# Kernel optimization log

Measured on AMD Instinct MI355X. Metric: run time of the kernel, lower is better.

## Reference

```python
import jax, jax.numpy as jnp
import numpy as np

N = 100000   # num nodes
E = 640000   # num edges
IN, H, OUT = 6, 128, 1
BN_EPS = 1e-5


def setup_inputs() -> dict:
    key = jax.random.key(0)
    ks = jax.random.split(key, 12)
    x = jax.random.normal(ks[0], (N, IN), dtype=jnp.float32)
    edge_index = jax.random.randint(ks[1], (2, E), 0, N, dtype=jnp.int64)
    def lin(k, fin, fout):
        s = 1.0 / np.sqrt(fin)
        return jax.random.uniform(k, (fin, fout), jnp.float32, -s, s)
    return {
        "x": x,
        "edge_index": edge_index,
        "W1": lin(ks[2], IN, H),  "b1": jnp.zeros((H,), jnp.float32),
        "W2": lin(ks[3], H, H),   "b2": jnp.zeros((H,), jnp.float32),
        "W3": lin(ks[4], H, OUT), "b3": jnp.zeros((OUT,), jnp.float32),
        "g1": jnp.ones((H,), jnp.float32),  "be1": jnp.zeros((H,), jnp.float32),
        "g2": jnp.ones((H,), jnp.float32),  "be2": jnp.zeros((H,), jnp.float32),
    }


def _gcn_norm(edge_index):
    # add self-loops, then symmetric normalization D^-1/2 (A+I) D^-1/2
    loop = jnp.arange(N, dtype=edge_index.dtype)
    src = jnp.concatenate([edge_index[0], loop])
    dst = jnp.concatenate([edge_index[1], loop])
    deg = jax.ops.segment_sum(jnp.ones_like(dst, dtype=jnp.float32), dst, num_segments=N)
    dis = jnp.where(deg > 0, jax.lax.rsqrt(deg), 0.0)
    norm = dis[src] * dis[dst]  # (E+N,)
    return src, dst, norm


def _conv(h, W, b, src, dst, norm):
    m = h @ W                                   # (N, out) linear transform first
    msg = m[src] * norm[:, None]                # gather + edge scaling
    return jax.ops.segment_sum(msg, dst, num_segments=N) + b


def _bn(h, g, be):
    mu = h.mean(axis=0)
    var = h.var(axis=0)  # biased, as torch BN uses for normalization
    return g * (h - mu) * jax.lax.rsqrt(var + BN_EPS) + be


def reference(x, edge_index, W1, b1, W2, b2, W3, b3, g1, be1, g2, be2):
    src, dst, norm = _gcn_norm(edge_index)
    h = jax.nn.relu(_bn(_conv(x, W1, b1, src, dst, norm), g1, be1))
    h = jax.nn.relu(_bn(_conv(h, W2, b2, src, dst, norm), g2, be2))
    out = _conv(h, W3, b3, src, dst, norm)
    return jax.nn.sigmoid(out)  # (N, 1) risk scores
```

## Files before the change

### kernel.cpp

```cpp
#include <hip/hip_runtime.h>
#include <hip/hip_bf16.h>
#include <math.h>

#define HDIM 128
#define BN_EPS 1e-5f
#define CHUNK 512
#define TM 64
#define LDA 132

__device__ __forceinline__ int eget(const void* ei, long long pos, int is64) {
    return is64 ? (int)((const long long*)ei)[pos] : ((const int*)ei)[pos];
}
__device__ __forceinline__ unsigned short f2bf(float f) {
    unsigned int u = __float_as_uint(f);
    u += 0x7fffu + ((u >> 16) & 1u);
    return (unsigned short)(u >> 16);
}
__device__ __forceinline__ float bflo(unsigned int u) {
    return __uint_as_float(u << 16);
}
__device__ __forceinline__ float bfhi(unsigned int u) {
    return __uint_as_float(u & 0xffff0000u);
}

__global__ void k_detect(const int* ei32, int* flag) {
    if (threadIdx.x == 0) {
        int nz = 0;
        for (int k = 0; k < 64; ++k) nz += (ei32[2 * k + 1] != 0);
        *flag = (nz < 8) ? 1 : 0;
    }
}

__global__ void k_count(const void* ei, const int* flag, int* cnt, int E) {
    int e = blockIdx.x * blockDim.x + threadIdx.x;
    if (e < E) {
        int d = eget(ei, (long long)E + e, *flag);
        atomicAdd(&cnt[d], 1);
    }
}

__global__ void k_dis(const int* cnt, float* dis, int N) {
    int i = blockIdx.x * blockDim.x + threadIdx.x;
    if (i < N) dis[i] = rsqrtf((float)(cnt[i] + 1));
}

__global__ void k_scan1(const int* cnt, int* bsum, int N) {
    __shared__ int s[256];
    int t = threadIdx.x;
    int i = blockIdx.x * CHUNK + t;
    int v = 0;
    if (i < N) v += cnt[i];
    if (i + 256 < N && t + 256 < CHUNK) v += cnt[i + 256];
    s[t] = v; __syncthreads();
    for (int o = 128; o > 0; o >>= 1) {
        if (t < o) s[t] += s[t + o];
        __syncthreads();
    }
    if (t == 0) bsum[blockIdx.x] = s[0];
}

__global__ void k_scan2(int* bsum, int nb) {
    __shared__ int s[512];
    int t = threadIdx.x;
    int carry = 0;
    for (int base = 0; base < nb; base += 512) {
        int i = base + t;
        int v = (i < nb) ? bsum[i] : 0;
        s[t] = v; __syncthreads();
        for (int o = 1; o < 512; o <<= 1) {
            int add = (t >= o) ? s[t - o] : 0;
            __syncthreads();
            s[t] += add;
            __syncthreads();
        }
        if (i < nb) bsum[i] = carry + s[t] - v;
        carry += s[511];
        __syncthreads();
    }
}

__global__ void k_scan3(const int* cnt, const int* bsum, int* rowptr, int N) {
    __shared__ int s[CHUNK];
    int t = threadIdx.x;
    int i = blockIdx.x * CHUNK + t;
    int v = (i < N) ? cnt[i] : 0;
    s[t] = v; __syncthreads();
    for (int o = 1; o < CHUNK; o <<= 1) {
        int add = (t >= o) ? s[t - o] : 0;
        __syncthreads();
        s[t] += add;
        __syncthreads();
    }
    if (i < N) rowptr[i] = bsum[blockIdx.x] + s[t] - v;
    if (i == N - 1) rowptr[N] = bsum[blockIdx.x] + s[t];
}

__global__ void k_fillcsr(const void* ei, const int* flag, const float* dis,
                          const int* rowptr, int* fill, int* esrc, float* enorm, int E) {
    int e = blockIdx.x * blockDim.x + threadIdx.x;
    if (e < E) {
        int is64 = *flag;
        int s = eget(ei, e, is64);
        int d = eget(ei, (long long)E + e, is64);
        int pos = rowptr[d] + atomicAdd(&fill[d], 1);
        esrc[pos] = s;
        enorm[pos] = dis[s] * dis[d];
    }
}

__global__ void k_padx(const float* __restrict__ x, float* __restrict__ xp, int N) {
    int t = blockIdx.x * blockDim.x + threadIdx.x;
    if (t < N * 8) {
        int i = t >> 3, c = t & 7;
        xp[t] = (c < 6) ? x[i * 6 + c] : 0.f;
    }
}

__global__ void k_gath_x(const float* __restrict__ xp, const int* __restrict__ rowptr,
                         const int* __restrict__ esrc, const float* __restrict__ enorm,
                         const float* __restrict__ dis, float* __restrict__ aggx, int N) {
    int i = blockIdx.x * blockDim.x + threadIdx.x;
    if (i >= N) return;
    float d = dis[i], d2 = d * d;
    float4 A = *(const float4*)&xp[i * 8];
    float2 B = *(const float2*)&xp[i * 8 + 4];
    float a0 = A.x * d2, a1 = A.y * d2, a2 = A.z * d2;
    float a3 = A.w * d2, a4 = B.x * d2, a5 = B.y * d2;
    int p = rowptr[i], pe = rowptr[i + 1];
    for (; p + 2 <= pe; p += 2) {
        int s0 = esrc[p], s1 = esrc[p + 1];
        float n0 = enorm[p], n1 = enorm[p + 1];
        float4 A0 = *(const float4*)&xp[s0 * 8];
        float2 B0 = *(const float2*)&xp[s0 * 8 + 4];
        float4 A1 = *(const float4*)&xp[s1 * 8];
        float2 B1 = *(const float2*)&xp[s1 * 8 + 4];
        a0 += A0.x * n0 + A1.x * n1; a1 += A0.y * n0 + A1.y * n1;
        a2 += A0.z * n0 + A1.z * n1; a3 += A0.w * n0 + A1.w * n1;
        a4 += B0.x * n0 + B1.x * n1; a5 += B0.y * n0 + B1.y * n1;
    }
    if (p < pe) {
        int s0 = esrc[p]; float n0 = enorm[p];
        float4 A0 = *(const float4*)&xp[s0 * 8];
        float2 B0 = *(const float2*)&xp[s0 * 8 + 4];
        a0 += A0.x * n0; a1 += A0.y * n0; a2 += A0.z * n0;
        a3 += A0.w * n0; a4 += B0.x * n0; a5 += B0.y * n0;
    }
    aggx[i * 6 + 0] = a0; aggx[i * 6 + 1] = a1; aggx[i * 6 + 2] = a2;
    aggx[i * 6 + 3] = a3; aggx[i * 6 + 4] = a4; aggx[i * 6 + 5] = a5;
}

__global__ void k_gemm6(const float* __restrict__ aggx, const float* __restrict__ W1,
                        const float* __restrict__ b1, unsigned short* __restrict__ out,
                        float* __restrict__ S, int N) {
    __shared__ float w[6 * HDIM];
    __shared__ float bb[HDIM];
    __shared__ float sh1[256], sh2[256];
    for (int t = threadIdx.x; t < 6 * HDIM; t += blockDim.x) w[t] = W1[t];
    if (threadIdx.x < HDIM) bb[threadIdx.x] = b1[threadIdx.x];
    __syncthreads();
    int j = threadIdx.x & (HDIM - 1);
    int sub = threadIdx.x >> 7;
    float s1 = 0.f, s2 = 0.f;
    for (long long i = blockIdx.x * 2 + sub; i < N; i += (long long)gridDim.x * 2) {
        const float* r = &aggx[i * 6];
        float acc = bb[j];
        acc += r[0] * w[0 * HDIM + j];
        acc += r[1] * w[1 * HDIM + j];
        acc += r[2] * w[2 * HDIM + j];
        acc += r[3] * w[3 * HDIM + j];
        acc += r[4] * w[4 * HDIM + j];
        acc += r[5] * w[5 * HDIM + j];
        out[i * HDIM + j] = f2bf(acc);
        s1 += acc; s2 += acc * acc;
    }
    sh1[threadIdx.x] = s1; sh2[threadIdx.x] = s2;
    __syncthreads();
    if (threadIdx.x < HDIM) {
        atomicAdd(&S[j], sh1[j] + sh1[j + HDIM]);
        atomicAdd(&S[HDIM + j], sh2[j] + sh2[j + HDIM]);
    }
}

__global__ void k_bnparams(const float* S, const float* g, const float* be,
                           float invN, float* P) {
    int j = threadIdx.x;
    if (j < HDIM) {
        float mu = S[j] * invN;
        float var = S[HDIM + j] * invN - mu * mu;
        float a = g[j] * rsqrtf(var + BN_EPS);
        P[j] = a;
        P[HDIM + j] = be[j] - mu * a;
    }
}

__global__ __launch_bounds__(512, 6)
void k_agg_gemm(const unsigned short* __restrict__ m1, const float* __restrict__ P1,
                const int* __restrict__ rowptr, const int* __restrict__ esrc,
                const float* __restrict__ enorm, const float* __restrict__ dis,
                const float* __restrict__ W, const float* __restrict__ b,
                float* __restrict__ out, float* __restrict__ S,
                int* __restrict__ ticket, int ntiles, int N) {
    __shared__ float At[TM * LDA];
    __shared__ int s_tile;
    const int tid = threadIdx.x;

    const int gl = tid & 31;
    const int gq = tid >> 5;
    const int c4 = gl * 4;
    const float4 pa = *(const float4*)&P1[c4];
    const float4 pb = *(const float4*)&P1[HDIM + c4];

    const int cg = tid & 31;
    const int rg = tid >> 5;
    const int c0 = cg * 4;
    const int r0 = rg * 4;
    const float4 bv = *(const float4*)&b[c0];

    for (;;) {
        if (tid == 0) s_tile = atomicAdd(ticket, 1);
        __syncthreads();
        const int tile = s_tile;
        if (tile >= ntiles) return;
        const long long i0 = (long long)tile * TM;

        for (int nn = gq; nn < TM; nn += 16) {
            long long i = i0 + nn;
            float a0 = 0.f, a1 = 0.f, a2 = 0.f, a3 = 0.f;
            if (i < N) {
                float d = dis[i], d2 = d * d;
                uint2 us = *(const uint2*)&m1[i * HDIM + c4];
                a0 = fmaxf(fmaf(pa.x, bflo(us.x), pb.x), 0.f) * d2;
                a1 = fmaxf(fmaf(pa.y, bfhi(us.x), pb.y), 0.f) * d2;
                a2 = fmaxf(fmaf(pa.z, bflo(us.y), pb.z), 0.f) * d2;
                a3 = fmaxf(fmaf(pa.w, bfhi(us.y), pb.w), 0.f) * d2;
                int p = rowptr[i], pe = rowptr[i + 1];
                for (; p + 2 <= pe; p += 2) {
                    int sA = esrc[p], sB = esrc[p + 1];
                    float nA = enorm[p], nB = enorm[p + 1];
                    uint2 uA = *(const uint2*)&m1[(long long)sA * HDIM + c4];
                    uint2 uB = *(const uint2*)&m1[(long long)sB * HDIM + c4];
                    a0 += fmaxf(fmaf(pa.x, bflo(uA.x), pb.x), 0.f) * nA
                        + fmaxf(fmaf(pa.x, bflo(uB.x), pb.x), 0.f) * nB;
                    a1 += fmaxf(fmaf(pa.y, bfhi(uA.x), pb.y), 0.f) * nA
                        + fmaxf(fmaf(pa.y, bfhi(uB.x), pb.y), 0.f) * nB;
                    a2 += fmaxf(fmaf(pa.z, bflo(uA.y), pb.z), 0.f) * nA
                        + fmaxf(fmaf(pa.z, bflo(uB.y), pb.z), 0.f) * nB;
                    a3 += fmaxf(fmaf(pa.w, bfhi(uA.y), pb.w), 0.f) * nA
                        + fmaxf(fmaf(pa.w, bfhi(uB.y), pb.w), 0.f) * nB;
                }
                if (p < pe) {
                    int sA = esrc[p]; float nA = enorm[p];
                    uint2 uA = *(const uint2*)&m1[(long long)sA * HDIM + c4];
                    a0 += fmaxf(fmaf(pa.x, bflo(uA.x), pb.x), 0.f) * nA;
                    a1 += fmaxf(fmaf(pa.y, bfhi(uA.x), pb.y), 0.f) * nA;
                    a2 += fmaxf(fmaf(pa.z, bflo(uA.y), pb.z), 0.f) * nA;
                    a3 += fmaxf(fmaf(pa.w, bfhi(uA.y), pb.w), 0.f) * nA;
                }
            }
            *(float4*)&At[nn * LDA + c4] = make_float4(a0, a1, a2, a3);
        }
        __syncthreads();

        float acc[4][4];
        #pragma unroll
        for (int rr = 0; rr < 4; ++rr) {
            acc[rr][0] = bv.x; acc[rr][1] = bv.y; acc[rr][2] = bv.z; acc[rr][3] = bv.w;
        }
        for (int k = 0; k < HDIM; k += 4) {
            const float4 w0 = *(const float4*)&W[(k + 0) * HDIM + c0];
            const float4 w1 = *(const float4*)&W[(k + 1) * HDIM + c0];
            const float4 w2 = *(const float4*)&W[(k + 2) * HDIM + c0];
            const float4 w3 = *(const float4*)&W[(k + 3) * HDIM + c0];
            #pragma unroll
            for (int rr = 0; rr < 4; ++rr) {
                const float4 av = *(const float4*)&At[(r0 + rr) * LDA + k];
                acc[rr][0] = fmaf(av.x, w0.x, acc[rr][0]);
                acc[rr][1] = fmaf(av.x, w0.y, acc[rr][1]);
                acc[rr][2] = fmaf(av.x, w0.z, acc[rr][2]);
                acc[rr][3] = fmaf(av.x, w0.w, acc[rr][3]);
                acc[rr][0] = fmaf(av.y, w1.x, acc[rr][0]);
                acc[rr][1] = fmaf(av.y, w1.y, acc[rr][1]);
                acc[rr][2] = fmaf(av.y, w1.z, acc[rr][2]);
                acc[rr][3] = fmaf(av.y, w1.w, acc[rr][3]);
                acc[rr][0] = fmaf(av.z, w2.x, acc[rr][0]);
                acc[rr][1] = fmaf(av.z, w2.y, acc[rr][1]);
                acc[rr][2] = fmaf(av.z, w2.z, acc[rr][2]);
                acc[rr][3] = fmaf(av.z, w2.w, acc[rr][3]);
                acc[rr][0] = fmaf(av.w, w3.x, acc[rr][0]);
                acc[rr][1] = fmaf(av.w, w3.y, acc[rr][1]);
                acc[rr][2] = fmaf(av.w, w3.z, acc[rr][2]);
                acc[rr][3] = fmaf(av.w, w3.w, acc[rr][3]);
            }
        }

        float cs1[4] = {0.f, 0.f, 0.f, 0.f};
        float cs2[4] = {0.f, 0.f, 0.f, 0.f};
        #pragma unroll
        for (int rr = 0; rr < 4; ++rr) {
            long long i = i0 + r0 + rr;
            if (i < N) {
                *(float4*)&out[i * HDIM + c0] =
                    make_float4(acc[rr][0], acc[rr][1], acc[rr][2], acc[rr][3]);
                #pragma unroll
                for (int cc = 0; cc < 4; ++cc) {
                    float v = acc[rr][cc];
                    cs1[cc] += v; cs2[cc] += v * v;
                }
            }
        }
        __syncthreads();
        #pragma unroll
        for (int cc = 0; cc < 4; ++cc) {
            At[rg * HDIM + c0 + cc]        = cs1[cc];
            At[2048 + rg * HDIM + c0 + cc] = cs2[cc];
        }
        __syncthreads();
        if (tid < 256) {
            int j = tid & (HDIM - 1);
            int which = tid >> 7;
            const float* bp = &At[which * 2048 + j];
            float s = 0.f;
            #pragma unroll
            for (int g = 0; g < 16; ++g) s += bp[g * HDIM];
            atomicAdd(&S[which * HDIM + j], s);
        }
        __syncthreads();
    }
}

__global__ void k_gemv2(const float* __restrict__ A, const float* __restrict__ P,
                        const float* __restrict__ W3, float* __restrict__ m3, int N) {
    int l = threadIdx.x & 31;
    int row = blockIdx.x * 8 + (threadIdx.x >> 5);
    if (row < N) {
        int c4 = l * 4;
        float4 pa = *(const float4*)&P[c4];
        float4 pb = *(const float4*)&P[HDIM + c4];
        float4 w  = *(const float4*)&W3[c4];
        float4 v  = *(const float4*)&A[(long long)row * HDIM + c4];
        float s = fmaxf(fmaf(pa.x, v.x, pb.x), 0.f) * w.x
                + fmaxf(fmaf(pa.y, v.y, pb.y), 0.f) * w.y
                + fmaxf(fmaf(pa.z, v.z, pb.z), 0.f) * w.z
                + fmaxf(fmaf(pa.w, v.w, pb.w), 0.f) * w.w;
        for (int o = 16; o > 0; o >>= 1) s += __shfl_down(s, o, 32);
        if (l == 0) m3[row] = s;
    }
}

__global__ void k_gath_o(const float* __restrict__ m3, const int* __restrict__ rowptr,
                         const int* __restrict__ esrc, const float* __restrict__ enorm,
                         const float* __restrict__ dis, const float* __restrict__ b3,
                         float* __restrict__ out, int N) {
    int i = blockIdx.x * blockDim.x + threadIdx.x;
    if (i < N) {
        float d = dis[i];
        float acc = m3[i] * d * d;
        int p = rowptr[i], pe = rowptr[i + 1];
        for (; p + 4 <= pe; p += 4) {
            float v0 = m3[esrc[p]]     * enorm[p];
            float v1 = m3[esrc[p + 1]] * enorm[p + 1];
            float v2 = m3[esrc[p + 2]] * enorm[p + 2];
            float v3 = m3[esrc[p + 3]] * enorm[p + 3];
            acc += (v0 + v1) + (v2 + v3);
        }
        for (; p < pe; ++p)
            acc += m3[esrc[p]] * enorm[p];
        acc += b3[0];
        out[i] = 1.f / (1.f + expf(-acc));
    }
}

extern "C" void kernel_launch(void* const* d_in, const int* in_sizes, int n_in,
                              void* d_out, int out_size, void* d_ws, size_t ws_size,
                              hipStream_t stream) {
    const float* x  = (const float*)d_in[0];
    const void*  ei = d_in[1];
    const float* W1 = (const float*)d_in[2];
    const float* b1 = (const float*)d_in[3];
    const float* W2 = (const float*)d_in[4];
    const float* b2 = (const float*)d_in[5];
    const float* W3 = (const float*)d_in[6];
    const float* b3 = (const float*)d_in[7];
    const float* g1 = (const float*)d_in[8];
    const float* be1 = (const float*)d_in[9];
    const float* g2 = (const float*)d_in[10];
    const float* be2 = (const float*)d_in[11];

    const int N = in_sizes[0] / 6;
    const int E = in_sizes[1] / 2;
    const float invN = 1.0f / (float)N;

    float* ws = (float*)d_ws;
    long long off = 0;
    auto pad4 = [](long long v) { return (v + 3) & ~3LL; };
    int*   flag   = (int*)ws;                 off += 16;
    int*   ticket = (int*)ws + 1;
    float* dis    = ws + off;                 off = pad4(off + N);
    int*   cnt    = (int*)(ws + off);         off = pad4(off + N);
    int*   rowptr = (int*)(ws + off);         off = pad4(off + N + 16);
    int*   esrc   = (int*)(ws + off);         off = pad4(off + E);
    float* enorm  = ws + off;                 off = pad4(off + E);
    int*   bsum   = (int*)(ws + off);         off += 512;
    float* S1     = ws + off;                 off += 256;
    float* S2     = ws + off;                 off += 256;
    float* P1     = ws + off;                 off += 256;
    float* P2     = ws + off;                 off += 256;
    float* xp     = ws + off;                 off = pad4(off + (long long)8 * N);
    float* aggx   = ws + off;                 off = pad4(off + (long long)6 * N);
    float* m3     = ws + off;                 off = pad4(off + N);
    unsigned short* m1 = (unsigned short*)(ws + off); off = pad4(off + (long long)64 * N);
    float* Hb2    = ws + off;                 off += (long long)HDIM * N;

    const int T = 256;
    const int bN  = (N + T - 1) / T;
    const int bE  = (E + T - 1) / T;
    const int nchunk = (N + CHUNK - 1) / CHUNK;
    const int ntiles = (N + TM - 1) / TM;

    hipMemsetAsync(flag, 0, 64, stream);
    hipMemsetAsync(S1, 0, 512 * sizeof(float), stream);
    k_detect<<<1, 64, 0, stream>>>((const int*)ei, flag);
    hipMemsetAsync(cnt, 0, (size_t)N * sizeof(int), stream);
    k_count<<<bE, T, 0, stream>>>(ei, flag, cnt, E);
    k_dis<<<bN, T, 0, stream>>>(cnt, dis, N);
    k_scan1<<<nchunk, 256, 0, stream>>>(cnt, bsum, N);
    k_scan2<<<1, 512, 0, stream>>>(bsum, nchunk);
    k_scan3<<<nchunk, CHUNK, 0, stream>>>(cnt, bsum, rowptr, N);
    hipMemsetAsync(cnt, 0, (size_t)N * sizeof(int), stream);
    k_fillcsr<<<bE, T, 0, stream>>>(ei, flag, dis, rowptr, cnt, esrc, enorm, E);

    k_padx<<<(N * 8 + T - 1) / T, T, 0, stream>>>(x, xp, N);
    k_gath_x<<<bN, T, 0, stream>>>(xp, rowptr, esrc, enorm, dis, aggx, N);
    k_gemm6<<<512, T, 0, stream>>>(aggx, W1, b1, m1, S1, N);
    k_bnparams<<<1, 128, 0, stream>>>(S1, g1, be1, invN, P1);

    k_agg_gemm<<<1024, 512, 0, stream>>>(m1, P1, rowptr, esrc, enorm, dis,
                                         W2, b2, Hb2, S2, ticket, ntiles, N);
    k_bnparams<<<1, 128, 0, stream>>>(S2, g2, be2, invN, P2);

    k_gemv2<<<(N + 7) / 8, T, 0, stream>>>(Hb2, P2, W3, m3, N);
    k_gath_o<<<bN, T, 0, stream>>>(m3, rowptr, esrc, enorm, dis, b3, (float*)d_out, N);
}
```

Baseline: 286.8 us.

## Fold BN param kernels into consumers, store layer-2 output as bf16, unroll gathers

Removes the two single-block k_bnparams launches by computing the BN scale and shift in shared memory at the start of k_agg_gemm and k_gemv2. The layer-2 activation buffer is now stored as bf16 instead of fp32, halving its write and read traffic, at some cost in precision. The edge-gather loops in k_gath_x and k_agg_gemm are unrolled to four edges so more independent loads are in flight. k_gemv2 now uses a fixed grid-stride launch.

```diff
diff --git a/kernel.cpp b/kernel.cpp
--- a/kernel.cpp
+++ b/kernel.cpp
@@ -15,6 +15,9 @@
     unsigned int u = __float_as_uint(f);
     u += 0x7fffu + ((u >> 16) & 1u);
     return (unsigned short)(u >> 16);
+}
+__device__ __forceinline__ unsigned int pack2bf(float lo, float hi) {
+    return (unsigned int)f2bf(lo) | ((unsigned int)f2bf(hi) << 16);
 }
 __device__ __forceinline__ float bflo(unsigned int u) {
     return __uint_as_float(u << 16);
@@ -127,18 +130,25 @@
     float a0 = A.x * d2, a1 = A.y * d2, a2 = A.z * d2;
     float a3 = A.w * d2, a4 = B.x * d2, a5 = B.y * d2;
     int p = rowptr[i], pe = rowptr[i + 1];
-    for (; p + 2 <= pe; p += 2) {
-        int s0 = esrc[p], s1 = esrc[p + 1];
-        float n0 = enorm[p], n1 = enorm[p + 1];
+    for (; p + 4 <= pe; p += 4) {
+        int s0 = esrc[p], s1 = esrc[p + 1], s2 = esrc[p + 2], s3 = esrc[p + 3];
+        float n0 = enorm[p], n1 = enorm[p + 1], n2 = enorm[p + 2], n3 = enorm[p + 3];
         float4 A0 = *(const float4*)&xp[s0 * 8];
         float2 B0 = *(const float2*)&xp[s0 * 8 + 4];
         float4 A1 = *(const float4*)&xp[s1 * 8];
         float2 B1 = *(const float2*)&xp[s1 * 8 + 4];
-        a0 += A0.x * n0 + A1.x * n1; a1 += A0.y * n0 + A1.y * n1;
-        a2 += A0.z * n0 + A1.z * n1; a3 += A0.w * n0 + A1.w * n1;
-        a4 += B0.x * n0 + B1.x * n1; a5 += B0.y * n0 + B1.y * n1;
-    }
-    if (p < pe) {
+        float4 A2 = *(const float4*)&xp[s2 * 8];
+        float2 B2 = *(const float2*)&xp[s2 * 8 + 4];
+        float4 A3 = *(const float4*)&xp[s3 * 8];
+        float2 B3 = *(const float2*)&xp[s3 * 8 + 4];
+        a0 += (A0.x * n0 + A1.x * n1) + (A2.x * n2 + A3.x * n3);
+        a1 += (A0.y * n0 + A1.y * n1) + (A2.y * n2 + A3.y * n3);
+        a2 += (A0.z * n0 + A1.z * n1) + (A2.z * n2 + A3.z * n3);
+        a3 += (A0.w * n0 + A1.w * n1) + (A2.w * n2 + A3.w * n3);
+        a4 += (B0.x * n0 + B1.x * n1) + (B2.x * n2 + B3.x * n3);
+        a5 += (B0.y * n0 + B1.y * n1) + (B2.y * n2 + B3.y * n3);
+    }
+    for (; p < pe; ++p) {
         int s0 = esrc[p]; float n0 = enorm[p];
         float4 A0 = *(const float4*)&xp[s0 * 8];
         float2 B0 = *(const float2*)&xp[s0 * 8 + 4];
@@ -181,34 +191,34 @@
     }
 }
 
-__global__ void k_bnparams(const float* S, const float* g, const float* be,
-                           float invN, float* P) {
-    int j = threadIdx.x;
-    if (j < HDIM) {
-        float mu = S[j] * invN;
-        float var = S[HDIM + j] * invN - mu * mu;
-        float a = g[j] * rsqrtf(var + BN_EPS);
-        P[j] = a;
-        P[HDIM + j] = be[j] - mu * a;
-    }
-}
-
 __global__ __launch_bounds__(512, 6)
-void k_agg_gemm(const unsigned short* __restrict__ m1, const float* __restrict__ P1,
+void k_agg_gemm(const unsigned short* __restrict__ m1,
+                const float* __restrict__ S1, const float* __restrict__ g1,
+                const float* __restrict__ be1, float invN,
                 const int* __restrict__ rowptr, const int* __restrict__ esrc,
                 const float* __restrict__ enorm, const float* __restrict__ dis,
                 const float* __restrict__ W, const float* __restrict__ b,
-                float* __restrict__ out, float* __restrict__ S,
+                unsigned short* __restrict__ out, float* __restrict__ S,
                 int* __restrict__ ticket, int ntiles, int N) {
     __shared__ float At[TM * LDA];
+    __shared__ float Pp[256];
     __shared__ int s_tile;
     const int tid = threadIdx.x;
+
+    if (tid < HDIM) {
+        float mu = S1[tid] * invN;
+        float var = S1[HDIM + tid] * invN - mu * mu;
+        float al = g1[tid] * rsqrtf(var + BN_EPS);
+        Pp[tid] = al;
+        Pp[HDIM + tid] = be1[tid] - mu * al;
+    }
+    __syncthreads();
 
     const int gl = tid & 31;
     const int gq = tid >> 5;
     const int c4 = gl * 4;
-    const float4 pa = *(const float4*)&P1[c4];
-    const float4 pb = *(const float4*)&P1[HDIM + c4];
+    const float4 pa = *(const float4*)&Pp[c4];
+    const float4 pb = *(const float4*)&Pp[HDIM + c4];
 
     const int cg = tid & 31;
     const int rg = tid >> 5;
@@ -234,7 +244,33 @@
                 a2 = fmaxf(fmaf(pa.z, bflo(us.y), pb.z), 0.f) * d2;
                 a3 = fmaxf(fmaf(pa.w, bfhi(us.y), pb.w), 0.f) * d2;
                 int p = rowptr[i], pe = rowptr[i + 1];
-                for (; p + 2 <= pe; p += 2) {
+                for (; p + 4 <= pe; p += 4) {
+                    int sA = esrc[p],     sB = esrc[p + 1];
+                    int sC = esrc[p + 2], sD = esrc[p + 3];
+                    float nA = enorm[p],     nB = enorm[p + 1];
+                    float nC = enorm[p + 2], nD = enorm[p + 3];
+                    uint2 uA = *(const uint2*)&m1[(long long)sA * HDIM + c4];
+                    uint2 uB = *(const uint2*)&m1[(long long)sB * HDIM + c4];
+                    uint2 uC = *(const uint2*)&m1[(long long)sC * HDIM + c4];
+                    uint2 uD = *(const uint2*)&m1[(long long)sD * HDIM + c4];
+                    a0 += (fmaxf(fmaf(pa.x, bflo(uA.x), pb.x), 0.f) * nA
+                         + fmaxf(fmaf(pa.x, bflo(uB.x), pb.x), 0.f) * nB)
+                        + (fmaxf(fmaf(pa.x, bflo(uC.x), pb.x), 0.f) * nC
+                         + fmaxf(fmaf(pa.x, bflo(uD.x), pb.x), 0.f) * nD);
+                    a1 += (fmaxf(fmaf(pa.y, bfhi(uA.x), pb.y), 0.f) * nA
+                         + fmaxf(fmaf(pa.y, bfhi(uB.x), pb.y), 0.f) * nB)
+                        + (fmaxf(fmaf(pa.y, bfhi(uC.x), pb.y), 0.f) * nC
+                         + fmaxf(fmaf(pa.y, bfhi(uD.x), pb.y), 0.f) * nD);
+                    a2 += (fmaxf(fmaf(pa.z, bflo(uA.y), pb.z), 0.f) * nA
+                         + fmaxf(fmaf(pa.z, bflo(uB.y), pb.z), 0.f) * nB)
+                        + (fmaxf(fmaf(pa.z, bflo(uC.y), pb.z), 0.f) * nC
+                         + fmaxf(fmaf(pa.z, bflo(uD.y), pb.z), 0.f) * nD);
+                    a3 += (fmaxf(fmaf(pa.w, bfhi(uA.y), pb.w), 0.f) * nA
+                         + fmaxf(fmaf(pa.w, bfhi(uB.y), pb.w), 0.f) * nB)
+                        + (fmaxf(fmaf(pa.w, bfhi(uC.y), pb.w), 0.f) * nC
+                         + fmaxf(fmaf(pa.w, bfhi(uD.y), pb.w), 0.f) * nD);
+                }
+                if (p + 2 <= pe) {
                     int sA = esrc[p], sB = esrc[p + 1];
                     float nA = enorm[p], nB = enorm[p + 1];
                     uint2 uA = *(const uint2*)&m1[(long long)sA * HDIM + c4];
@@ -247,6 +283,7 @@
                         + fmaxf(fmaf(pa.z, bflo(uB.y), pb.z), 0.f) * nB;
                     a3 += fmaxf(fmaf(pa.w, bfhi(uA.y), pb.w), 0.f) * nA
                         + fmaxf(fmaf(pa.w, bfhi(uB.y), pb.w), 0.f) * nB;
+                    p += 2;
                 }
                 if (p < pe) {
                     int sA = esrc[p]; float nA = enorm[p];
@@ -299,8 +336,10 @@
         for (int rr = 0; rr < 4; ++rr) {
             long long i = i0 + r0 + rr;
             if (i < N) {
-                *(float4*)&out[i * HDIM + c0] =
-                    make_float4(acc[rr][0], acc[rr][1], acc[rr][2], acc[rr][3]);
+                uint2 o;
+                o.x = pack2bf(acc[rr][0], acc[rr][1]);
+                o.y = pack2bf(acc[rr][2], acc[rr][3]);
+                *(uint2*)&out[i * HDIM + c0] = o;
                 #pragma unroll
                 for (int cc = 0; cc < 4; ++cc) {
                     float v = acc[rr][cc];
@@ -328,20 +367,32 @@
     }
 }
 
-__global__ void k_gemv2(const float* __restrict__ A, const float* __restrict__ P,
+__global__ void k_gemv2(const unsigned short* __restrict__ m2,
+                        const float* __restrict__ S2, const float* __restrict__ g2,
+                        const float* __restrict__ be2, float invN,
                         const float* __restrict__ W3, float* __restrict__ m3, int N) {
-    int l = threadIdx.x & 31;
-    int row = blockIdx.x * 8 + (threadIdx.x >> 5);
-    if (row < N) {
-        int c4 = l * 4;
-        float4 pa = *(const float4*)&P[c4];
-        float4 pb = *(const float4*)&P[HDIM + c4];
-        float4 w  = *(const float4*)&W3[c4];
-        float4 v  = *(const float4*)&A[(long long)row * HDIM + c4];
-        float s = fmaxf(fmaf(pa.x, v.x, pb.x), 0.f) * w.x
-                + fmaxf(fmaf(pa.y, v.y, pb.y), 0.f) * w.y
-                + fmaxf(fmaf(pa.z, v.z, pb.z), 0.f) * w.z
-                + fmaxf(fmaf(pa.w, v.w, pb.w), 0.f) * w.w;
+    __shared__ float Pp[256];
+    int tid = threadIdx.x;
+    if (tid < HDIM) {
+        float mu = S2[tid] * invN;
+        float var = S2[HDIM + tid] * invN - mu * mu;
+        float al = g2[tid] * rsqrtf(var + BN_EPS);
+        Pp[tid] = al;
+        Pp[HDIM + tid] = be2[tid] - mu * al;
+    }
+    __syncthreads();
+    int l = tid & 31;
+    int c4 = l * 4;
+    float4 pa = *(const float4*)&Pp[c4];
+    float4 pb = *(const float4*)&Pp[HDIM + c4];
+    float4 w  = *(const float4*)&W3[c4];
+    for (long long row = blockIdx.x * 8 + (tid >> 5); row < N;
+         row += (long long)gridDim.x * 8) {
+        uint2 v = *(const uint2*)&m2[row * HDIM + c4];
+        float s = fmaxf(fmaf(pa.x, bflo(v.x), pb.x), 0.f) * w.x
+                + fmaxf(fmaf(pa.y, bfhi(v.x), pb.y), 0.f) * w.y
+                + fmaxf(fmaf(pa.z, bflo(v.y), pb.z), 0.f) * w.z
+                + fmaxf(fmaf(pa.w, bfhi(v.y), pb.w), 0.f) * w.w;
         for (int o = 16; o > 0; o >>= 1) s += __shfl_down(s, o, 32);
         if (l == 0) m3[row] = s;
     }
@@ -403,13 +454,11 @@
     int*   bsum   = (int*)(ws + off);         off += 512;
     float* S1     = ws + off;                 off += 256;
     float* S2     = ws + off;                 off += 256;
-    float* P1     = ws + off;                 off += 256;
-    float* P2     = ws + off;                 off += 256;
     float* xp     = ws + off;                 off = pad4(off + (long long)8 * N);
     float* aggx   = ws + off;                 off = pad4(off + (long long)6 * N);
     float* m3     = ws + off;                 off = pad4(off + N);
     unsigned short* m1 = (unsigned short*)(ws + off); off = pad4(off + (long long)64 * N);
-    float* Hb2    = ws + off;                 off += (long long)HDIM * N;
+    unsigned short* m2 = (unsigned short*)(ws + off); off = pad4(off + (long long)64 * N);
 
     const int T = 256;
     const int bN  = (N + T - 1) / T;
@@ -432,12 +481,11 @@
     k_padx<<<(N * 8 + T - 1) / T, T, 0, stream>>>(x, xp, N);
     k_gath_x<<<bN, T, 0, stream>>>(xp, rowptr, esrc, enorm, dis, aggx, N);
     k_gemm6<<<512, T, 0, stream>>>(aggx, W1, b1, m1, S1, N);
-    k_bnparams<<<1, 128, 0, stream>>>(S1, g1, be1, invN, P1);
-
-    k_agg_gemm<<<1024, 512, 0, stream>>>(m1, P1, rowptr, esrc, enorm, dis,
-                                         W2, b2, Hb2, S2, ticket, ntiles, N);
-    k_bnparams<<<1, 128, 0, stream>>>(S2, g2, be2, invN, P2);
-
-    k_gemv2<<<(N + 7) / 8, T, 0, stream>>>(Hb2, P2, W3, m3, N);
+
+    k_agg_gemm<<<1024, 512, 0, stream>>>(m1, S1, g1, be1, invN,
+                                         rowptr, esrc, enorm, dis,
+                                         W2, b2, m2, S2, ticket, ntiles, N);
+
+    k_gemv2<<<1024, T, 0, stream>>>(m2, S2, g2, be2, invN, W3, m3, N);
     k_gath_o<<<bN, T, 0, stream>>>(m3, rowptr, esrc, enorm, dis, b3, (float*)d_out, N);
 }
```

New measurement: 276.7 us. 1.04x faster.
